# Optimization experiments

Hardware: AMD Instinct MI355X
Metric: run time of the kernel (lower is better)

## Reference

```python
import jax, jax.numpy as jnp
import numpy as np

B, S, D, H, DH, FF = 2, 2048, 1024, 16, 64, 4096
EPS = 1e-6


def setup_inputs() -> dict:
    key = jax.random.key(0)
    ks = jax.random.split(key, 12)
    s = lambda fan: 1.0 / np.sqrt(fan)
    return {
        "x": jax.random.normal(ks[0], (B, S, D), dtype=jnp.float32),
        "mask": jax.random.randint(ks[1], (B, S), 0, 2).astype(bool),
        "Wq": jax.random.normal(ks[2], (D, H * DH), dtype=jnp.float32) * s(D),
        "Wk": jax.random.normal(ks[3], (D, H * DH), dtype=jnp.float32) * s(D),
        "Wv": jax.random.normal(ks[4], (D, H * DH), dtype=jnp.float32) * s(D),
        "Wo": jax.random.normal(ks[5], (H * DH, D), dtype=jnp.float32) * s(H * DH),
        "bo": jnp.zeros((D,), dtype=jnp.float32),
        "W1": jax.random.normal(ks[6], (D, FF), dtype=jnp.float32) * s(D),
        "b1": jnp.zeros((FF,), dtype=jnp.float32),
        "W2": jax.random.normal(ks[7], (FF, D), dtype=jnp.float32) * s(FF),
        "b2": jnp.zeros((D,), dtype=jnp.float32),
        "g1": jnp.ones((D,), dtype=jnp.float32),   # layer_norm1 target_std
        "m1": jnp.zeros((D,), dtype=jnp.float32),  # layer_norm1 target_mean
        "g2": jnp.ones((D,), dtype=jnp.float32),
        "m2": jnp.zeros((D,), dtype=jnp.float32),
    }


def layer_norm(x, g, m):
    mu = jnp.mean(x, axis=-1, keepdims=True)
    xc = x - mu
    std = jnp.sqrt(jnp.mean(xc * xc, axis=-1, keepdims=True) + EPS)
    return g * xc / std + m


def reference(x, mask, Wq, Wk, Wv, Wo, bo, W1, b1, W2, b2, g1, m1, g2, m2):
    # --- multi-head self-attention (no proj bias) ---
    q = (x @ Wq).reshape(B, S, H, DH)
    k = (x @ Wk).reshape(B, S, H, DH)
    v = (x @ Wv).reshape(B, S, H, DH)
    scores = jnp.einsum("bqhd,bkhd->bhqk", q, k) / np.sqrt(DH)  # [B,H,S,S]
    scores = jnp.where(mask[:, None, None, :], -jnp.inf, scores)
    att = jax.nn.softmax(scores, axis=-1)
    ctx = jnp.einsum("bhqk,bkhd->bqhd", att, v).reshape(B, S, H * DH)
    attn_out = ctx @ Wo + bo
    # --- post-LN residual block (pre_ln=False, dropouts=0 in eval) ---
    x1 = layer_norm(attn_out + x, g1, m1)
    ff = jax.nn.relu(x1 @ W1 + b1) @ W2 + b2
    return layer_norm(ff + x1, g2, m2)
```

## Files before the change

### kernel.cpp

```cpp
#include <hip/hip_runtime.h>
#include <hip/hip_bf16.h>


typedef __bf16 bf16;
typedef __bf16 bf16x8 __attribute__((ext_vector_type(8)));
typedef __bf16 bf16x4 __attribute__((ext_vector_type(4)));
typedef float  f32x4  __attribute__((ext_vector_type(4)));
typedef float  f32x16 __attribute__((ext_vector_type(16)));
typedef unsigned u32x2 __attribute__((ext_vector_type(2)));
typedef unsigned u32x4 __attribute__((ext_vector_type(4)));

#define DEVI __device__ __forceinline__

constexpr int S_LEN  = 2048;
constexpr int NTOK   = 4096;
constexpr int DMODEL = 1024;
constexpr int NFF    = 4096;
constexpr float SCALE2 = 0.125f * 1.44269504088896f;
constexpr float MASKV2 = -30000.0f;

DEVI void gld16(const void* g, void* l) {
  __builtin_amdgcn_global_load_lds((const __attribute__((address_space(1))) void*)g,
                                   (__attribute__((address_space(3))) void*)l, 16, 0, 0);
}

DEVI f32x4 mfma16(bf16x8 a, bf16x8 b, f32x4 c) {
  return __builtin_amdgcn_mfma_f32_16x16x32_bf16(a, b, c, 0, 0, 0);
}
DEVI f32x16 mfma32(bf16x8 a, bf16x8 b, f32x16 c) {
  return __builtin_amdgcn_mfma_f32_32x32x16_bf16(a, b, c, 0, 0, 0);
}
DEVI unsigned cvtpk(float lo, float hi) {
  unsigned d;
  asm("v_cvt_pk_bf16_f32 %0, %1, %2" : "=v"(d) : "v"(lo), "v"(hi));
  return d;
}
DEVI void plswap(unsigned &a, unsigned &b) {
#if __has_builtin(__builtin_amdgcn_permlane32_swap)
  u32x2 r = __builtin_amdgcn_permlane32_swap(a, b, false, false);
  a = r[0]; b = r[1];
#else
  asm volatile("v_permlane32_swap_b32 %0, %1" : "+v"(a), "+v"(b));
#endif
}
DEVI float fexp2(float x) {
#if __has_builtin(__builtin_amdgcn_exp2f)
  return __builtin_amdgcn_exp2f(x);
#else
  return exp2f(x);
#endif
}

template <int MODE>
__global__ __launch_bounds__(256) void gemm_bt(
    const bf16* __restrict__ A, const bf16* __restrict__ Bt,
    void* __restrict__ out, const float* __restrict__ bias,
    int M, int N, int ld, int Kc)
{
  __shared__ bf16 As[128 * 32];
  __shared__ bf16 Bs[128 * 32];
  const int tid  = threadIdx.x;
  const int lane = tid & 63, w = tid >> 6;
  const int wr = w >> 1, wc = w & 1;
  const int brow = blockIdx.y * 128, bcol = blockIdx.x * 128;
  const int kz = blockIdx.z;

  const bf16* Ag = A  + (size_t)(brow + w * 32 + (lane >> 2)) * ld + kz * Kc + (lane & 3) * 8;
  const bf16* Bg = Bt + (size_t)(bcol + w * 32 + (lane >> 2)) * ld + kz * Kc + (lane & 3) * 8;
  bf16* AsW = As + w * 1024;
  bf16* BsW = Bs + w * 1024;

  f32x4 acc[4][4] = {};

  for (int k0 = 0; k0 < Kc; k0 += 32) {
    gld16(Ag + k0,                    AsW);
    gld16(Ag + k0 + (size_t)16 * ld,  AsW + 512);
    gld16(Bg + k0,                    BsW);
    gld16(Bg + k0 + (size_t)16 * ld,  BsW + 512);
    __syncthreads();

    bf16x8 af[4], bfr[4];
#pragma unroll
    for (int m = 0; m < 4; ++m)
      af[m] = *(const bf16x8*)&As[(wr * 64 + m * 16 + (lane & 15)) * 32 + (lane >> 4) * 8];
#pragma unroll
    for (int n = 0; n < 4; ++n)
      bfr[n] = *(const bf16x8*)&Bs[(wc * 64 + n * 16 + (lane & 15)) * 32 + (lane >> 4) * 8];
#pragma unroll
    for (int m = 0; m < 4; ++m)
#pragma unroll
      for (int n = 0; n < 4; ++n)
        acc[m][n] = mfma16(af[m], bfr[n], acc[m][n]);
    __syncthreads();
  }

  const size_t plane = (size_t)NTOK * DMODEL;
#pragma unroll
  for (int m = 0; m < 4; ++m)
#pragma unroll
    for (int n = 0; n < 4; ++n)
#pragma unroll
      for (int r = 0; r < 4; ++r) {
        const int row = brow + wr * 64 + m * 16 + (lane >> 4) * 4 + r;
        const int col = bcol + wc * 64 + n * 16 + (lane & 15);
        const float v = acc[m][n][r];
        if (MODE == 0) {
          const int b = row >> 11, s = row & 2047;
          const int which = col >> 10, c = col & 1023, h = c >> 6, d = c & 63;
          bf16* qkv = (bf16*)out;
          if (which == 0)
            qkv[(((size_t)(b * 16 + h)) * 2048 + s) * 64 + d] = (bf16)v;
          else if (which == 1)
            (qkv + plane)[(((size_t)(b * 16 + h)) * 2048 + s) * 64 + d] = (bf16)v;
          else
            (qkv + 2 * plane)[(((size_t)(b * 16 + h)) * 64 + d) * 2048 + s] = (bf16)v;
        } else if (MODE == 3) {
          const float t = v + bias[col];
          ((bf16*)out)[(size_t)row * N + col] = (bf16)fmaxf(t, 0.0f);
        } else {
          ((float*)out)[(size_t)kz * M * N + (size_t)row * N + col] = v;
        }
      }
}

__global__ __launch_bounds__(512) void attn_k(
    const bf16* __restrict__ q, const bf16* __restrict__ k,
    const bf16* __restrict__ vt, const unsigned* __restrict__ mbits,
    bf16* __restrict__ ctx)
{
  __shared__ __align__(16) char smem[36864];
  bf16* Kl = (bf16*)smem;
  bf16* Vl = (bf16*)(smem + 16384);
  const int tid = threadIdx.x, lane = tid & 63, w = tid >> 6;
  const int hi = lane >> 5, li = lane & 31;
  const int bh = blockIdx.y, b = bh >> 4, h = bh & 15;
  const int qbase = blockIdx.x * 256 + w * 32;

  bf16x8 qf[4];
  {
    const bf16* qp = q + ((size_t)bh * S_LEN + qbase + li) * 64 + hi * 8;
#pragma unroll
    for (int c = 0; c < 4; ++c) qf[c] = *(const bf16x8*)(qp + c * 16);
  }

  f32x16 o[2] = {};
  float mrun = -3.0e38f, lrun = 0.f;

  const int srow = w * 8 + (lane >> 3);
  const int sslot = (lane & 7) ^ ((srow ^ (srow >> 3)) & 7);
  const bf16* kg = k  + ((size_t)bh * S_LEN + srow) * 64 + sslot * 8;
  const bf16* vg = vt + ((size_t)bh * 64 + srow) * S_LEN + sslot * 8;

  gld16(kg, Kl + w * 512);
  gld16(vg, Vl + w * 512);
  __syncthreads();

  int buf = 0;
  for (int kt = 0; kt < 32; ++kt) {
    const int nb = buf ^ 1;
    if (kt + 1 < 32) {
      gld16(kg + (size_t)(kt + 1) * 4096, Kl + nb * 4096 + w * 512);
      gld16(vg + (kt + 1) * 64,           Vl + nb * 4096 + w * 512);
    }
    const unsigned mw0 = mbits[b * 64 + kt * 2]     >> (hi * 4);
    const unsigned mw1 = mbits[b * 64 + kt * 2 + 1] >> (hi * 4);
    const bf16* Kb = Kl + buf * 4096;
    const bf16* Vb = Vl + buf * 4096;

    float sc[2][16];
#pragma unroll
    for (int kblk = 0; kblk < 2; ++kblk) {
      const int key = kblk * 32 + li;
      const unsigned swb = ((key ^ (key >> 3)) & 7) << 4;
      const char* kr = (const char*)Kb + key * 128;
      f32x16 st = {};
#pragma unroll
      for (int c = 0; c < 4; ++c) {
        const bf16x8 kf = *(const bf16x8*)(kr + ((unsigned)(c * 32 + hi * 16) ^ swb));
        st = mfma32(kf, qf[c], st);
      }
      const unsigned msh = kblk ? mw1 : mw0;
#pragma unroll
      for (int r = 0; r < 16; ++r) {
        const int cb = (r & 3) + 8 * (r >> 2);
        const float v = st[r] * SCALE2;
        sc[kblk][r] = (msh & (1u << cb)) ? MASKV2 : v;
      }
    }

    float tm = fmaxf(sc[0][0], sc[1][0]);
#pragma unroll
    for (int r = 1; r < 16; ++r) tm = fmaxf(tm, fmaxf(sc[0][r], sc[1][r]));
    tm = fmaxf(tm, __shfl_xor(tm, 32, 64));
    const float mnew = fmaxf(mrun, tm);
    const float alpha = fexp2(mrun - mnew);
    mrun = mnew;
    float rsum = 0.f;
#pragma unroll
    for (int kblk = 0; kblk < 2; ++kblk)
#pragma unroll
      for (int r = 0; r < 16; ++r) {
        const float p = fexp2(sc[kblk][r] - mnew);
        sc[kblk][r] = p;
        rsum += p;
      }
    rsum += __shfl_xor(rsum, 32, 64);
    lrun = lrun * alpha + rsum;
    o[0] *= alpha;
    o[1] *= alpha;

    bf16x8 pa[4];
#pragma unroll
    for (int kblk = 0; kblk < 2; ++kblk)
#pragma unroll
      for (int hf = 0; hf < 2; ++hf) {
        unsigned A = cvtpk(sc[kblk][hf * 8 + 0], sc[kblk][hf * 8 + 1]);
        unsigned B = cvtpk(sc[kblk][hf * 8 + 2], sc[kblk][hf * 8 + 3]);
        unsigned C = cvtpk(sc[kblk][hf * 8 + 4], sc[kblk][hf * 8 + 5]);
        unsigned D = cvtpk(sc[kblk][hf * 8 + 6], sc[kblk][hf * 8 + 7]);
        plswap(A, C);
        plswap(B, D);
        const u32x4 t = {A, B, C, D};
        pa[kblk * 2 + hf] = __builtin_bit_cast(bf16x8, t);
      }

#pragma unroll
    for (int dblk = 0; dblk < 2; ++dblk) {
      const int d = dblk * 32 + li;
      const unsigned swb = ((d ^ (d >> 3)) & 7) << 4;
      const char* vr = (const char*)Vb + d * 128;
#pragma unroll
      for (int ch = 0; ch < 4; ++ch) {
        const bf16x8 vf = *(const bf16x8*)(vr + ((unsigned)(ch * 32 + hi * 16) ^ swb));
        o[dblk] = mfma32(vf, pa[ch], o[dblk]);
      }
    }
    __syncthreads();
    buf = nb;
  }

  const float rl = 1.0f / lrun;
  char* Ep = smem + w * 4608;
#pragma unroll
  for (int dblk = 0; dblk < 2; ++dblk)
#pragma unroll
    for (int g = 0; g < 4; ++g) {
      const unsigned lo = cvtpk(o[dblk][4 * g + 0] * rl, o[dblk][4 * g + 1] * rl);
      const unsigned hw = cvtpk(o[dblk][4 * g + 2] * rl, o[dblk][4 * g + 3] * rl);
      const int d0 = 8 * g + 4 * hi + 32 * dblk;
      *(unsigned long long*)(Ep + li * 144 + d0 * 2) =
          ((unsigned long long)hw << 32) | (unsigned long long)lo;
    }
#pragma unroll
  for (int i = 0; i < 4; ++i) {
    const int r = (lane >> 3) + 8 * i;
    const bf16x8 vv = *(const bf16x8*)(Ep + r * 144 + (lane & 7) * 16);
    *(bf16x8*)(ctx + ((size_t)b * S_LEN + qbase + r) * DMODEL + h * 64 + (lane & 7) * 8) = vv;
  }
}

template <int NPART>
__global__ __launch_bounds__(256) void ln_k(
    const float* __restrict__ parts, const float* __restrict__ bias,
    const float* __restrict__ resid, const float* __restrict__ gam,
    const float* __restrict__ bet, float* __restrict__ of, bf16* __restrict__ ob)
{
  const int row = blockIdx.x, t = threadIdx.x;
  float4 v = ((const float4*)(parts + (size_t)row * DMODEL))[t];
#pragma unroll
  for (int p = 1; p < NPART; ++p) {
    const float4 u = ((const float4*)(parts + ((size_t)p * NTOK + row) * DMODEL))[t];
    v.x += u.x; v.y += u.y; v.z += u.z; v.w += u.w;
  }
  {
    const float4 b4 = ((const float4*)bias)[t];
    const float4 r4 = ((const float4*)(resid + (size_t)row * DMODEL))[t];
    v.x += b4.x + r4.x; v.y += b4.y + r4.y; v.z += b4.z + r4.z; v.w += b4.w + r4.w;
  }
  float s  = v.x + v.y + v.z + v.w;
  float s2 = v.x * v.x + v.y * v.y + v.z * v.z + v.w * v.w;
#pragma unroll
  for (int off = 1; off < 64; off <<= 1) {
    s  += __shfl_xor(s, off, 64);
    s2 += __shfl_xor(s2, off, 64);
  }
  __shared__ float ps[4], ps2[4];
  if ((t & 63) == 0) { ps[t >> 6] = s; ps2[t >> 6] = s2; }
  __syncthreads();
  s  = ps[0] + ps[1] + ps[2] + ps[3];
  s2 = ps2[0] + ps2[1] + ps2[2] + ps2[3];
  const float mu   = s * (1.f / 1024.f);
  const float var  = fmaxf(s2 * (1.f / 1024.f) - mu * mu, 0.f);
  const float rstd = rsqrtf(var + 1e-6f);
  const float4 g4 = ((const float4*)gam)[t];
  const float4 b4 = ((const float4*)bet)[t];
  float4 ov;
  ov.x = g4.x * (v.x - mu) * rstd + b4.x;
  ov.y = g4.y * (v.y - mu) * rstd + b4.y;
  ov.z = g4.z * (v.z - mu) * rstd + b4.z;
  ov.w = g4.w * (v.w - mu) * rstd + b4.w;
  if (of) ((float4*)(of + (size_t)row * DMODEL))[t] = ov;
  if (ob) {
    const bf16x4 o4 = {(bf16)ov.x, (bf16)ov.y, (bf16)ov.z, (bf16)ov.w};
    *(bf16x4*)(ob + (size_t)row * DMODEL + t * 4) = o4;
  }
}

__global__ __launch_bounds__(256) void f2b_k(const float* __restrict__ in,
                                             bf16* __restrict__ out, int n4)
{
  const int i = blockIdx.x * 256 + threadIdx.x;
  if (i >= n4) return;
  const float4 v = ((const float4*)in)[i];
  const bf16x4 o = {(bf16)v.x, (bf16)v.y, (bf16)v.z, (bf16)v.w};
  *(bf16x4*)(out + (size_t)i * 4) = o;
}

__global__ __launch_bounds__(256) void tconv_k(const float* __restrict__ in,
                                               bf16* __restrict__ out, int K, int N)
{
  __shared__ float tile[32][33];
  const int tx = threadIdx.x & 31, ty = threadIdx.x >> 5;
  const int r0 = blockIdx.y * 32, c0 = blockIdx.x * 32;
#pragma unroll
  for (int i = 0; i < 32; i += 8)
    tile[ty + i][tx] = in[(size_t)(r0 + ty + i) * N + c0 + tx];
  __syncthreads();
#pragma unroll
  for (int i = 0; i < 32; i += 8)
    out[(size_t)(c0 + ty + i) * K + r0 + tx] = (bf16)tile[tx][ty + i];
}

__global__ __launch_bounds__(256) void mask_conv_k(const void* __restrict__ m,
                                                   unsigned* __restrict__ mbits)
{
  __shared__ int s_gt1, s_f1;
  const int t = threadIdx.x;
  if (t == 0) { s_gt1 = 0; s_f1 = 0; }
  __syncthreads();
  const unsigned int* wds = (const unsigned int*)m;
  int gt1 = 0, f1 = 0;
  for (int i = t; i < 1024; i += 256) {
    const unsigned int x = wds[i];
    gt1 |= (x > 1u);
    f1  |= (x == 0x3F800000u);
  }
  if (gt1) atomicOr(&s_gt1, 1);
  if (f1)  atomicOr(&s_f1, 1);
  __syncthreads();
  const int md = s_f1 ? 2 : (s_gt1 ? 1 : 0);
  if (t < NTOK / 32) {
    unsigned wd = 0;
    for (int j = 0; j < 32; ++j) {
      const int e = t * 32 + j;
      unsigned mv;
      if (md == 1)      mv = (((const unsigned char*)m)[e] != 0);
      else if (md == 2) mv = (((const float*)m)[e] != 0.f);
      else              mv = (((const int*)m)[e] != 0);
      wd |= mv << j;
    }
    mbits[t] = wd;
  }
}

extern "C" void kernel_launch(void* const* d_in, const int* in_sizes, int n_in,
                              void* d_out, int out_size, void* d_ws, size_t ws_size,
                              hipStream_t stream)
{
  const float* x    = (const float*)d_in[0];
  const void*  mask = d_in[1];
  const float* Wq   = (const float*)d_in[2];
  const float* Wk   = (const float*)d_in[3];
  const float* Wv   = (const float*)d_in[4];
  const float* Wo   = (const float*)d_in[5];
  const float* bo   = (const float*)d_in[6];
  const float* W1   = (const float*)d_in[7];
  const float* b1   = (const float*)d_in[8];
  const float* W2   = (const float*)d_in[9];
  const float* b2   = (const float*)d_in[10];
  const float* g1   = (const float*)d_in[11];
  const float* m1   = (const float*)d_in[12];
  const float* g2   = (const float*)d_in[13];
  const float* m2   = (const float*)d_in[14];

  const size_t plane = (size_t)NTOK * DMODEL;
  const int split = (ws_size >= (size_t)140 * 1024 * 1024) ? 4 : 2;

  char* ws = (char*)d_ws;
  size_t off = 0;
  auto alloc = [&](size_t bytes) {
    char* p = ws + off;
    off += (bytes + 255) & ~(size_t)255;
    return p;
  };
  char* region0 = alloc((size_t)16 * 1024 * 1024 + 1024);
  bf16* xb     = (bf16*)region0;
  bf16* WqkvT  = (bf16*)(region0 + plane * 2);
  bf16* WoT    = (bf16*)(region0 + plane * 2 + (size_t)3 * DMODEL * DMODEL * 2);
  float* x1    = (float*)region0;

  bf16* W1T  = (bf16*)alloc((size_t)NFF * DMODEL * 2);
  bf16* W2T  = (bf16*)alloc((size_t)DMODEL * NFF * 2);
  bf16* qkv  = (bf16*)alloc(4 * plane * 2);
  bf16* qb = qkv, *kb = qkv + plane, *vtb = qkv + 2 * plane, *ctxb = qkv + 3 * plane;
  bf16* hb   = qkv;
  float* parts = (float*)alloc((size_t)split * plane * 4);
  bf16*  x1b   = (bf16*)alloc(plane * 2);
  unsigned* maskbits = (unsigned*)alloc(512);

  f2b_k<<<dim3(4096), dim3(256), 0, stream>>>(x, xb, NTOK * DMODEL / 4);
  tconv_k<<<dim3(32, 32),  dim3(256), 0, stream>>>(Wq, WqkvT, DMODEL, DMODEL);
  tconv_k<<<dim3(32, 32),  dim3(256), 0, stream>>>(Wk, WqkvT + (size_t)DMODEL * DMODEL, DMODEL, DMODEL);
  tconv_k<<<dim3(32, 32),  dim3(256), 0, stream>>>(Wv, WqkvT + (size_t)2 * DMODEL * DMODEL, DMODEL, DMODEL);
  tconv_k<<<dim3(32, 32),  dim3(256), 0, stream>>>(Wo, WoT, DMODEL, DMODEL);
  tconv_k<<<dim3(128, 32), dim3(256), 0, stream>>>(W1, W1T, DMODEL, NFF);
  tconv_k<<<dim3(32, 128), dim3(256), 0, stream>>>(W2, W2T, NFF, DMODEL);
  mask_conv_k<<<dim3(1), dim3(256), 0, stream>>>(mask, maskbits);

  gemm_bt<0><<<dim3(24, 32), dim3(256), 0, stream>>>(
      xb, WqkvT, qkv, nullptr, NTOK, 3 * DMODEL, DMODEL, DMODEL);

  attn_k<<<dim3(S_LEN / 256, 32), dim3(512), 0, stream>>>(qb, kb, vtb, maskbits, ctxb);

  gemm_bt<4><<<dim3(8, 32, 2), dim3(256), 0, stream>>>(
      ctxb, WoT, parts, nullptr, NTOK, DMODEL, DMODEL, DMODEL / 2);
  ln_k<2><<<dim3(NTOK), dim3(256), 0, stream>>>(parts, bo, x, g1, m1, x1, x1b);

  gemm_bt<3><<<dim3(32, 32), dim3(256), 0, stream>>>(
      x1b, W1T, hb, b1, NTOK, NFF, DMODEL, DMODEL);
  gemm_bt<4><<<dim3(8, 32, split), dim3(256), 0, stream>>>(
      hb, W2T, parts, nullptr, NTOK, DMODEL, NFF, NFF / split);
  if (split == 4)
    ln_k<4><<<dim3(NTOK), dim3(256), 0, stream>>>(parts, b2, x1, g2, m2, (float*)d_out, nullptr);
  else
    ln_k<2><<<dim3(NTOK), dim3(256), 0, stream>>>(parts, b2, x1, g2, m2, (float*)d_out, nullptr);
}
```

Baseline: 308.2 us.

## Remap GEMM blocks per XCD, raise MFMA wave priority, use bf16 residual in LN2

GEMM launches are flattened to 1D grids and block ids are remapped so that each XCD (id&7) owns a contiguous band of output rows. The intent is better L2 reuse of A tiles within each chiplet's cache. s_setprio is raised around the MFMA sequences in the GEMM and attention kernels to favour waves that are issuing matrix ops. The second layer norm now reads the residual x1 from its bf16 copy instead of writing and reading an fp32 x1, which saves traffic but adds rounding error to the residual path.

```diff
diff --git a/kernel.cpp b/kernel.cpp
--- a/kernel.cpp
+++ b/kernel.cpp
@@ -55,15 +55,22 @@
 __global__ __launch_bounds__(256) void gemm_bt(
     const bf16* __restrict__ A, const bf16* __restrict__ Bt,
     void* __restrict__ out, const float* __restrict__ bias,
-    int M, int N, int ld, int Kc)
+    int M, int N, int ld, int Kc, int nx, int ny)
 {
   __shared__ bf16 As[128 * 32];
   __shared__ bf16 Bs[128 * 32];
   const int tid  = threadIdx.x;
   const int lane = tid & 63, w = tid >> 6;
   const int wr = w >> 1, wc = w & 1;
-  const int brow = blockIdx.y * 128, bcol = blockIdx.x * 128;
-  const int kz = blockIdx.z;
+
+  const int id  = blockIdx.x;
+  const int xcd = id & 7;
+  int t2 = id >> 3;
+  const int bx = t2 % nx;  t2 /= nx;
+  const int ppx = ny >> 3;
+  const int kz = t2 / ppx;
+  const int by = xcd * ppx + (t2 % ppx);
+  const int brow = by * 128, bcol = bx * 128;
 
   const bf16* Ag = A  + (size_t)(brow + w * 32 + (lane >> 2)) * ld + kz * Kc + (lane & 3) * 8;
   const bf16* Bg = Bt + (size_t)(bcol + w * 32 + (lane >> 2)) * ld + kz * Kc + (lane & 3) * 8;
@@ -86,11 +93,13 @@
 #pragma unroll
     for (int n = 0; n < 4; ++n)
       bfr[n] = *(const bf16x8*)&Bs[(wc * 64 + n * 16 + (lane & 15)) * 32 + (lane >> 4) * 8];
+    __builtin_amdgcn_s_setprio(1);
 #pragma unroll
     for (int m = 0; m < 4; ++m)
 #pragma unroll
       for (int n = 0; n < 4; ++n)
         acc[m][n] = mfma16(af[m], bfr[n], acc[m][n]);
+    __builtin_amdgcn_s_setprio(0);
     __syncthreads();
   }
 
@@ -174,11 +183,13 @@
       const unsigned swb = ((key ^ (key >> 3)) & 7) << 4;
       const char* kr = (const char*)Kb + key * 128;
       f32x16 st = {};
+      __builtin_amdgcn_s_setprio(1);
 #pragma unroll
       for (int c = 0; c < 4; ++c) {
         const bf16x8 kf = *(const bf16x8*)(kr + ((unsigned)(c * 32 + hi * 16) ^ swb));
         st = mfma32(kf, qf[c], st);
       }
+      __builtin_amdgcn_s_setprio(0);
       const unsigned msh = kblk ? mw1 : mw0;
 #pragma unroll
       for (int r = 0; r < 16; ++r) {
@@ -229,11 +240,13 @@
       const int d = dblk * 32 + li;
       const unsigned swb = ((d ^ (d >> 3)) & 7) << 4;
       const char* vr = (const char*)Vb + d * 128;
+      __builtin_amdgcn_s_setprio(1);
 #pragma unroll
       for (int ch = 0; ch < 4; ++ch) {
         const bf16x8 vf = *(const bf16x8*)(vr + ((unsigned)(ch * 32 + hi * 16) ^ swb));
         o[dblk] = mfma32(vf, pa[ch], o[dblk]);
       }
+      __builtin_amdgcn_s_setprio(0);
     }
     __syncthreads();
     buf = nb;
@@ -259,10 +272,10 @@
   }
 }
 
-template <int NPART>
+template <int NPART, int RB>
 __global__ __launch_bounds__(256) void ln_k(
     const float* __restrict__ parts, const float* __restrict__ bias,
-    const float* __restrict__ resid, const float* __restrict__ gam,
+    const void* __restrict__ resid, const float* __restrict__ gam,
     const float* __restrict__ bet, float* __restrict__ of, bf16* __restrict__ ob)
 {
   const int row = blockIdx.x, t = threadIdx.x;
@@ -274,7 +287,13 @@
   }
   {
     const float4 b4 = ((const float4*)bias)[t];
-    const float4 r4 = ((const float4*)(resid + (size_t)row * DMODEL))[t];
+    float4 r4;
+    if (RB) {
+      const bf16x4 rb = *(const bf16x4*)((const bf16*)resid + (size_t)row * DMODEL + t * 4);
+      r4.x = (float)rb[0]; r4.y = (float)rb[1]; r4.z = (float)rb[2]; r4.w = (float)rb[3];
+    } else {
+      r4 = ((const float4*)((const float*)resid + (size_t)row * DMODEL))[t];
+    }
     v.x += b4.x + r4.x; v.y += b4.y + r4.y; v.z += b4.z + r4.z; v.w += b4.w + r4.w;
   }
   float s  = v.x + v.y + v.z + v.w;
@@ -397,7 +416,6 @@
   bf16* xb     = (bf16*)region0;
   bf16* WqkvT  = (bf16*)(region0 + plane * 2);
   bf16* WoT    = (bf16*)(region0 + plane * 2 + (size_t)3 * DMODEL * DMODEL * 2);
-  float* x1    = (float*)region0;
 
   bf16* W1T  = (bf16*)alloc((size_t)NFF * DMODEL * 2);
   bf16* W2T  = (bf16*)alloc((size_t)DMODEL * NFF * 2);
@@ -417,21 +435,21 @@
   tconv_k<<<dim3(32, 128), dim3(256), 0, stream>>>(W2, W2T, NFF, DMODEL);
   mask_conv_k<<<dim3(1), dim3(256), 0, stream>>>(mask, maskbits);
 
-  gemm_bt<0><<<dim3(24, 32), dim3(256), 0, stream>>>(
-      xb, WqkvT, qkv, nullptr, NTOK, 3 * DMODEL, DMODEL, DMODEL);
+  gemm_bt<0><<<dim3(768), dim3(256), 0, stream>>>(
+      xb, WqkvT, qkv, nullptr, NTOK, 3 * DMODEL, DMODEL, DMODEL, 24, 32);
 
   attn_k<<<dim3(S_LEN / 256, 32), dim3(512), 0, stream>>>(qb, kb, vtb, maskbits, ctxb);
 
-  gemm_bt<4><<<dim3(8, 32, 2), dim3(256), 0, stream>>>(
-      ctxb, WoT, parts, nullptr, NTOK, DMODEL, DMODEL, DMODEL / 2);
-  ln_k<2><<<dim3(NTOK), dim3(256), 0, stream>>>(parts, bo, x, g1, m1, x1, x1b);
-
-  gemm_bt<3><<<dim3(32, 32), dim3(256), 0, stream>>>(
-      x1b, W1T, hb, b1, NTOK, NFF, DMODEL, DMODEL);
-  gemm_bt<4><<<dim3(8, 32, split), dim3(256), 0, stream>>>(
-      hb, W2T, parts, nullptr, NTOK, DMODEL, NFF, NFF / split);
+  gemm_bt<4><<<dim3(512), dim3(256), 0, stream>>>(
+      ctxb, WoT, parts, nullptr, NTOK, DMODEL, DMODEL, DMODEL / 2, 8, 32);
+  ln_k<2, 0><<<dim3(NTOK), dim3(256), 0, stream>>>(parts, bo, x, g1, m1, nullptr, x1b);
+
+  gemm_bt<3><<<dim3(1024), dim3(256), 0, stream>>>(
+      x1b, W1T, hb, b1, NTOK, NFF, DMODEL, DMODEL, 32, 32);
+  gemm_bt<4><<<dim3(256 * split), dim3(256), 0, stream>>>(
+      hb, W2T, parts, nullptr, NTOK, DMODEL, NFF, NFF / split, 8, 32);
   if (split == 4)
-    ln_k<4><<<dim3(NTOK), dim3(256), 0, stream>>>(parts, b2, x1, g2, m2, (float*)d_out, nullptr);
+    ln_k<4, 1><<<dim3(NTOK), dim3(256), 0, stream>>>(parts, b2, x1b, g2, m2, (float*)d_out, nullptr);
   else
-    ln_k<2><<<dim3(NTOK), dim3(256), 0, stream>>>(parts, b2, x1, g2, m2, (float*)d_out, nullptr);
-}
+    ln_k<2, 1><<<dim3(NTOK), dim3(256), 0, stream>>>(parts, b2, x1b, g2, m2, (float*)d_out, nullptr);
+}
```

New measurement: 282.7 us. 1.09x faster.
